# Kernel optimization log

Measured on AMD Instinct MI355X. Metric: run time of the kernel, lower is better.

The kernel has to match this reference:

```python
import jax, jax.numpy as jnp
import numpy as np

B, C, TX, MAX_Y = 16, 192, 1024, 4096


def setup_inputs() -> dict:
    key = jax.random.key(0)
    k1, k2, k3, k4, k5 = jax.random.split(key, 5)
    return {
        "m_p": jax.random.normal(k1, (B, C, TX), dtype=jnp.float32),
        "logs_p": jax.random.normal(k2, (B, C, TX), dtype=jnp.float32),
        "logw": jax.random.normal(k3, (B, 1, TX), dtype=jnp.float32),
        "noise": jax.random.normal(k4, (B, C, MAX_Y), dtype=jnp.float32),
        "x_lengths": jax.random.randint(k5, (B,), 0, TX).astype(jnp.int32),
        "max_y": MAX_Y,
    }


def reference(m_p, logs_p, logw, noise, x_lengths, max_y):
    # m_p, logs_p: [B, C, Tx]; logw: [B, 1, Tx]; noise: [B, C, Ty]
    b, c, tx = m_p.shape
    dtype = m_p.dtype
    noise_scale = jnp.asarray(1.0, dtype)
    length_scale = jnp.asarray(1.0, dtype)

    x_len = jnp.maximum(x_lengths, 1)
    x_mask = (jnp.arange(tx)[None, :] < x_len[:, None]).astype(dtype)  # [B, Tx]

    # w = exp(logw) * x_mask * length_scale ; w_ceil = ceil(w)
    w_ceil = jnp.ceil(jnp.exp(logw[:, 0, :]) * x_mask * length_scale)  # [B, Tx]
    y_len = jnp.clip(jnp.sum(w_ceil, axis=1), 1, max_y).astype(jnp.int32)  # [B]
    y_mask = (jnp.arange(max_y)[None, :] < y_len[:, None]).astype(dtype)  # [B, Ty]

    # generate_path: monotonic alignment from cumulative durations
    cum = jnp.cumsum(w_ceil, axis=1)  # [B, Tx]
    ty = jnp.arange(max_y)
    seq = (ty[None, None, :] < cum[:, :, None]).astype(dtype)  # [B, Tx, Ty]
    path = seq - jnp.pad(seq, ((0, 0), (1, 0), (0, 0)))[:, :-1, :]  # per-token band
    attn = jnp.transpose(path, (0, 2, 1)) * x_mask[:, None, :] * y_mask[:, :, None]  # [B, Ty, Tx]

    # length regulation: expand stats to frame rate
    m_exp = jnp.einsum("byt,bct->bcy", attn, m_p)      # [B, C, Ty]
    logs_exp = jnp.einsum("byt,bct->bcy", attn, logs_p)  # [B, C, Ty]

    z_p = m_exp + noise * jnp.exp(logs_exp) * noise_scale
    return z_p, y_mask[:, None, :]
```

## Files before the change

### kernel.cpp

```cpp
#include <hip/hip_runtime.h>
#include <hip/hip_bf16.h>


__global__ void k_scan(const float* __restrict__ logw,
                       const int* __restrict__ x_lengths,
                       float* __restrict__ cum,
                       int* __restrict__ y_len,
                       int tx, int max_y) {
    int b = blockIdx.x;
    int t = threadIdx.x;
    __shared__ float s[1024];

    int xl = x_lengths[b];
    if (xl < 1) xl = 1;

    float w = 0.f;
    if (t < tx && t < xl) {
        w = ceilf(expf(logw[b * tx + t]));
    }
    s[t] = w;
    __syncthreads();

    for (int off = 1; off < 1024; off <<= 1) {
        float v = 0.f;
        if (t >= off) v = s[t - off];
        __syncthreads();
        if (t >= off) s[t] += v;
        __syncthreads();
    }

    if (t < tx) cum[b * tx + t] = s[t];
    if (t == 0) {
        float tot = s[tx - 1];
        float yl = fminf(fmaxf(tot, 1.f), (float)max_y);
        y_len[b] = (int)yl;
    }
}

__global__ void k_tmap(const float* __restrict__ cum,
                       const int* __restrict__ y_len,
                       int* __restrict__ tmap,
                       float* __restrict__ y_mask_out,
                       int tx, int max_y) {
    int b = blockIdx.y;
    int y = blockIdx.x * blockDim.x + threadIdx.x;
    if (y >= max_y) return;

    int yl = y_len[b];
    int t = -1;
    if (y < yl) {
        const float* c = cum + b * tx;
        float fy = (float)y;
        int lo = 0, hi = tx - 1;
        while (lo < hi) {
            int mid = (lo + hi) >> 1;
            if (c[mid] > fy) hi = mid; else lo = mid + 1;
        }
        t = lo;
    }
    tmap[b * max_y + y] = t;
    y_mask_out[b * max_y + y] = (y < yl) ? 1.f : 0.f;
}

__global__ void k_expand(const float* __restrict__ m_p,
                         const float* __restrict__ logs_p,
                         const float* __restrict__ noise,
                         const int* __restrict__ tmap,
                         float* __restrict__ z,
                         int C, int tx, int max_y) {
    int b = blockIdx.z;
    int c = blockIdx.y;
    int y = blockIdx.x * blockDim.x + threadIdx.x;
    if (y >= max_y) return;

    int t = tmap[b * max_y + y];
    float n = noise[(size_t)(b * C + c) * max_y + y];
    float out;
    if (t >= 0) {
        size_t idx = (size_t)(b * C + c) * tx + t;
        float m  = m_p[idx];
        float ls = logs_p[idx];
        out = m + n * expf(ls);
    } else {
        out = n;
    }
    z[(size_t)(b * C + c) * max_y + y] = out;
}

extern "C" void kernel_launch(void* const* d_in, const int* in_sizes, int n_in,
                              void* d_out, int out_size, void* d_ws, size_t ws_size,
                              hipStream_t stream) {
    const float* m_p    = (const float*)d_in[0];
    const float* logs_p = (const float*)d_in[1];
    const float* logw   = (const float*)d_in[2];
    const float* noise  = (const float*)d_in[3];
    const int*   x_len  = (const int*)  d_in[4];

    const int B    = in_sizes[4];
    const int TX   = in_sizes[2] / B;
    const int C    = in_sizes[0] / (B * TX);
    const int MAXY = in_sizes[3] / (B * C);

    float* z      = (float*)d_out;
    float* y_mask = (float*)d_out + (size_t)B * C * MAXY;

    float* cum  = (float*)d_ws;
    int*   ylen = (int*)(cum + (size_t)B * TX);
    int*   tmap = ylen + ((B + 63) & ~63);

    k_scan<<<dim3(B), dim3(1024), 0, stream>>>(logw, x_len, cum, ylen, TX, MAXY);

    k_tmap<<<dim3((MAXY + 255) / 256, B), dim3(256), 0, stream>>>(
        cum, ylen, tmap, y_mask, TX, MAXY);

    k_expand<<<dim3((MAXY + 255) / 256, C, B), dim3(256), 0, stream>>>(
        m_p, logs_p, noise, tmap, z, C, TX, MAXY);
}
```

Baseline: 154.8 us.

## Stage per-row stats and exp in LDS, vectorize expand over frames

Replaces the per-frame gather kernel with one block per (batch, channel) row that loads m_p and exp(logs_p) for the whole row into shared memory, then streams noise, the frame-to-token map and the output as float4 vectors. This computes the exponential once per source token rather than per output frame and replaces scattered global gathers with LDS lookups. It hardcodes a row length of 1024 (256 threads x float4) and assumes max_y divisible by 4.

```diff
diff --git a/kernel.cpp b/kernel.cpp
--- a/kernel.cpp
+++ b/kernel.cpp
@@ -62,29 +62,45 @@
     y_mask_out[b * max_y + y] = (y < yl) ? 1.f : 0.f;
 }
 
-__global__ void k_expand(const float* __restrict__ m_p,
-                         const float* __restrict__ logs_p,
-                         const float* __restrict__ noise,
-                         const int* __restrict__ tmap,
-                         float* __restrict__ z,
-                         int C, int tx, int max_y) {
-    int b = blockIdx.z;
-    int c = blockIdx.y;
-    int y = blockIdx.x * blockDim.x + threadIdx.x;
-    if (y >= max_y) return;
+__global__ void __launch_bounds__(256) k_expand2(
+        const float* __restrict__ m_p,
+        const float* __restrict__ logs_p,
+        const float* __restrict__ noise,
+        const int* __restrict__ tmap,
+        float* __restrict__ z,
+        int C, int tx, int max_y) {
+    __shared__ float sm[1024];
+    __shared__ float se[1024];
 
-    int t = tmap[b * max_y + y];
-    float n = noise[(size_t)(b * C + c) * max_y + y];
-    float out;
-    if (t >= 0) {
-        size_t idx = (size_t)(b * C + c) * tx + t;
-        float m  = m_p[idx];
-        float ls = logs_p[idx];
-        out = m + n * expf(ls);
-    } else {
-        out = n;
+    const int bc  = blockIdx.x;
+    const int b   = bc / C;
+    const int tid = threadIdx.x;
+
+    const float4* m4 = (const float4*)(m_p    + (size_t)bc * tx);
+    const float4* l4 = (const float4*)(logs_p + (size_t)bc * tx);
+    float4 mv = m4[tid];
+    float4 lv = l4[tid];
+    int j = tid * 4;
+    sm[j + 0] = mv.x; sm[j + 1] = mv.y; sm[j + 2] = mv.z; sm[j + 3] = mv.w;
+    se[j + 0] = expf(lv.x); se[j + 1] = expf(lv.y);
+    se[j + 2] = expf(lv.z); se[j + 3] = expf(lv.w);
+    __syncthreads();
+
+    const float4* n4 = (const float4*)(noise + (size_t)bc * max_y);
+    const int4*   t4 = (const int4*)  (tmap  + (size_t)b  * max_y);
+    float4*       z4 = (float4*)      (z     + (size_t)bc * max_y);
+
+    const int nvec = max_y >> 2;
+    for (int i = tid; i < nvec; i += 256) {
+        float4 n = n4[i];
+        int4   t = t4[i];
+        float4 o;
+        o.x = (t.x >= 0) ? fmaf(n.x, se[t.x], sm[t.x]) : n.x;
+        o.y = (t.y >= 0) ? fmaf(n.y, se[t.y], sm[t.y]) : n.y;
+        o.z = (t.z >= 0) ? fmaf(n.z, se[t.z], sm[t.z]) : n.z;
+        o.w = (t.w >= 0) ? fmaf(n.w, se[t.w], sm[t.w]) : n.w;
+        z4[i] = o;
     }
-    z[(size_t)(b * C + c) * max_y + y] = out;
 }
 
 extern "C" void kernel_launch(void* const* d_in, const int* in_sizes, int n_in,
@@ -113,6 +129,6 @@
     k_tmap<<<dim3((MAXY + 255) / 256, B), dim3(256), 0, stream>>>(
         cum, ylen, tmap, y_mask, TX, MAXY);
 
-    k_expand<<<dim3((MAXY + 255) / 256, C, B), dim3(256), 0, stream>>>(
+    k_expand2<<<dim3(B * C), dim3(256), 0, stream>>>(
         m_p, logs_p, noise, tmap, z, C, TX, MAXY);
 }
```

Measured after the change: 130.3 us. 15.8% less time.

## Fuse scan with tmap and stage expanded stats in shared memory

Applied to the files above, without the earlier changes.

Merges the cumulative-duration scan and the frame-to-token binary search into one kernel that searches the shared-memory prefix sums directly, removing one launch and the global cum/y_len round trip. The expand kernel now handles two channel rows per block. It preloads m_p and exp(logs_p) rows into LDS with float4 loads, then gathers from LDS with vectorized tmap, noise and z accesses. This cuts redundant exp calls and uncoalesced global gathers. In exchange the code hardcodes TX=1024 and MAX_Y=4096 (thread-to-element mapping) and requires even C.

```diff
diff --git a/kernel.cpp b/kernel.cpp
--- a/kernel.cpp
+++ b/kernel.cpp
@@ -2,22 +2,22 @@
 #include <hip/hip_bf16.h>
 
 
-__global__ void k_scan(const float* __restrict__ logw,
-                       const int* __restrict__ x_lengths,
-                       float* __restrict__ cum,
-                       int* __restrict__ y_len,
-                       int tx, int max_y) {
-    int b = blockIdx.x;
-    int t = threadIdx.x;
+__global__ void __launch_bounds__(1024) k_scan_tmap(
+        const float* __restrict__ logw,
+        const int* __restrict__ x_lengths,
+        int* __restrict__ tmap,
+        float* __restrict__ y_mask,
+        int tx, int max_y) {
+    const int b = blockIdx.x;
+    const int t = threadIdx.x;
     __shared__ float s[1024];
+    __shared__ int yl_sh;
 
     int xl = x_lengths[b];
     if (xl < 1) xl = 1;
 
     float w = 0.f;
-    if (t < tx && t < xl) {
-        w = ceilf(expf(logw[b * tx + t]));
-    }
+    if (t < xl) w = ceilf(expf(logw[b * tx + t]));
     s[t] = w;
     __syncthreads();
 
@@ -29,62 +29,94 @@
         __syncthreads();
     }
 
-    if (t < tx) cum[b * tx + t] = s[t];
-    if (t == 0) {
-        float tot = s[tx - 1];
-        float yl = fminf(fmaxf(tot, 1.f), (float)max_y);
-        y_len[b] = (int)yl;
+    if (t == 0)
+        yl_sh = (int)fminf(fmaxf(s[tx - 1], 1.f), (float)max_y);
+    __syncthreads();
+    const int yl = yl_sh;
+
+    const int y0 = t * 4;
+    int res[4];
+    float msk[4];
+#pragma unroll
+    for (int k = 0; k < 4; ++k) {
+        const int y = y0 + k;
+        int r = -1;
+        if (y < yl) {
+            float fy = (float)y;
+            int lo = 0, hi = tx - 1;
+            while (lo < hi) {
+                int mid = (lo + hi) >> 1;
+                if (s[mid] > fy) hi = mid; else lo = mid + 1;
+            }
+            r = lo;
+        }
+        res[k] = r;
+        msk[k] = (y < yl) ? 1.f : 0.f;
     }
+    ((int4*)(tmap + (size_t)b * max_y))[t] =
+        make_int4(res[0], res[1], res[2], res[3]);
+    ((float4*)(y_mask + (size_t)b * max_y))[t] =
+        make_float4(msk[0], msk[1], msk[2], msk[3]);
 }
 
-__global__ void k_tmap(const float* __restrict__ cum,
-                       const int* __restrict__ y_len,
-                       int* __restrict__ tmap,
-                       float* __restrict__ y_mask_out,
-                       int tx, int max_y) {
-    int b = blockIdx.y;
-    int y = blockIdx.x * blockDim.x + threadIdx.x;
-    if (y >= max_y) return;
+__global__ void __launch_bounds__(256) k_expand3(
+        const float* __restrict__ m_p,
+        const float* __restrict__ logs_p,
+        const float* __restrict__ noise,
+        const int* __restrict__ tmap,
+        float* __restrict__ z,
+        int C, int tx, int max_y) {
+    __shared__ float sm[2][1024];
+    __shared__ float se[2][1024];
 
-    int yl = y_len[b];
-    int t = -1;
-    if (y < yl) {
-        const float* c = cum + b * tx;
-        float fy = (float)y;
-        int lo = 0, hi = tx - 1;
-        while (lo < hi) {
-            int mid = (lo + hi) >> 1;
-            if (c[mid] > fy) hi = mid; else lo = mid + 1;
+    const int tid   = threadIdx.x;
+    const int chunk = blockIdx.x;
+    const int b     = chunk / (C >> 1);
+    const int c0    = (chunk - b * (C >> 1)) * 2;
+    const size_t row0 = (size_t)b * C + c0;
+
+#pragma unroll
+    for (int r = 0; r < 2; ++r) {
+        float4 mv = ((const float4*)(m_p    + (row0 + r) * tx))[tid];
+        float4 lv = ((const float4*)(logs_p + (row0 + r) * tx))[tid];
+        int j = tid * 4;
+        sm[r][j + 0] = mv.x; sm[r][j + 1] = mv.y;
+        sm[r][j + 2] = mv.z; sm[r][j + 3] = mv.w;
+        se[r][j + 0] = expf(lv.x); se[r][j + 1] = expf(lv.y);
+        se[r][j + 2] = expf(lv.z); se[r][j + 3] = expf(lv.w);
+    }
+    __syncthreads();
+
+    const int4* t4 = (const int4*)(tmap + (size_t)b * max_y);
+
+    int4   tv[4];
+    float4 nv[4][2];
+#pragma unroll
+    for (int it = 0; it < 4; ++it)
+        tv[it] = t4[tid + it * 256];
+#pragma unroll
+    for (int it = 0; it < 4; ++it) {
+        const int i = tid + it * 256;
+#pragma unroll
+        for (int r = 0; r < 2; ++r)
+            nv[it][r] = ((const float4*)(noise + (row0 + r) * max_y))[i];
+    }
+
+#pragma unroll
+    for (int it = 0; it < 4; ++it) {
+        const int i = tid + it * 256;
+        const int4 t = tv[it];
+#pragma unroll
+        for (int r = 0; r < 2; ++r) {
+            const float4 n = nv[it][r];
+            float4 o;
+            o.x = (t.x >= 0) ? fmaf(n.x, se[r][t.x], sm[r][t.x]) : n.x;
+            o.y = (t.y >= 0) ? fmaf(n.y, se[r][t.y], sm[r][t.y]) : n.y;
+            o.z = (t.z >= 0) ? fmaf(n.z, se[r][t.z], sm[r][t.z]) : n.z;
+            o.w = (t.w >= 0) ? fmaf(n.w, se[r][t.w], sm[r][t.w]) : n.w;
+            ((float4*)(z + (row0 + r) * max_y))[i] = o;
         }
-        t = lo;
     }
-    tmap[b * max_y + y] = t;
-    y_mask_out[b * max_y + y] = (y < yl) ? 1.f : 0.f;
-}
-
-__global__ void k_expand(const float* __restrict__ m_p,
-                         const float* __restrict__ logs_p,
-                         const float* __restrict__ noise,
-                         const int* __restrict__ tmap,
-                         float* __restrict__ z,
-                         int C, int tx, int max_y) {
-    int b = blockIdx.z;
-    int c = blockIdx.y;
-    int y = blockIdx.x * blockDim.x + threadIdx.x;
-    if (y >= max_y) return;
-
-    int t = tmap[b * max_y + y];
-    float n = noise[(size_t)(b * C + c) * max_y + y];
-    float out;
-    if (t >= 0) {
-        size_t idx = (size_t)(b * C + c) * tx + t;
-        float m  = m_p[idx];
-        float ls = logs_p[idx];
-        out = m + n * expf(ls);
-    } else {
-        out = n;
-    }
-    z[(size_t)(b * C + c) * max_y + y] = out;
 }
 
 extern "C" void kernel_launch(void* const* d_in, const int* in_sizes, int n_in,
@@ -104,15 +136,11 @@
     float* z      = (float*)d_out;
     float* y_mask = (float*)d_out + (size_t)B * C * MAXY;
 
-    float* cum  = (float*)d_ws;
-    int*   ylen = (int*)(cum + (size_t)B * TX);
-    int*   tmap = ylen + ((B + 63) & ~63);
+    int* tmap = (int*)d_ws;
 
-    k_scan<<<dim3(B), dim3(1024), 0, stream>>>(logw, x_len, cum, ylen, TX, MAXY);
+    k_scan_tmap<<<dim3(B), dim3(1024), 0, stream>>>(
+        logw, x_len, tmap, y_mask, TX, MAXY);
 
-    k_tmap<<<dim3((MAXY + 255) / 256, B), dim3(256), 0, stream>>>(
-        cum, ylen, tmap, y_mask, TX, MAXY);
-
-    k_expand<<<dim3((MAXY + 255) / 256, C, B), dim3(256), 0, stream>>>(
+    k_expand3<<<dim3(B * (C >> 1)), dim3(256), 0, stream>>>(
         m_p, logs_p, noise, tmap, z, C, TX, MAXY);
 }
```

Result: faster. 127.9 us (-17.3%).
